# Kernel tuning notes

Hardware: AMD Instinct MI355X
Metric: run time of the kernel (lower is better)

Reference implementation:

```python
import jax, jax.numpy as jnp
import numpy as np
import math

N_EMBD = 1024
HIDDEN = 4 * N_EMBD
N_EXPERTS = 8
TOP_K = 2
B, T = 4, 2048


def new_gelu(x):
    c = math.sqrt(2.0 / math.pi)
    return 0.5 * x * (1.0 + jnp.tanh(c * (x + 0.044715 * x * x * x)))


def setup_inputs() -> dict:
    key = jax.random.key(0)
    ks = jax.random.split(key, 10)
    s = 0.02
    return {
        "x": jax.random.normal(ks[0], (B, T, N_EMBD), dtype=jnp.float32),
        # shared expert (1 shared expert)
        "Wfc_s": jax.random.normal(ks[1], (N_EMBD, HIDDEN), dtype=jnp.float32) * s,
        "bfc_s": jnp.zeros((HIDDEN,), dtype=jnp.float32),
        "Wproj_s": jax.random.normal(ks[2], (HIDDEN, N_EMBD), dtype=jnp.float32) * s,
        "bproj_s": jnp.zeros((N_EMBD,), dtype=jnp.float32),
        # router (no bias)
        "Wr": jax.random.normal(ks[3], (N_EMBD, N_EXPERTS), dtype=jnp.float32) * s,
        # routed experts, stacked on leading expert dim
        "Wfc": jax.random.normal(ks[4], (N_EXPERTS, N_EMBD, HIDDEN), dtype=jnp.float32) * s,
        "bfc": jnp.zeros((N_EXPERTS, HIDDEN), dtype=jnp.float32),
        "Wproj": jax.random.normal(ks[5], (N_EXPERTS, HIDDEN, N_EMBD), dtype=jnp.float32) * s,
        "bproj": jnp.zeros((N_EXPERTS, N_EMBD), dtype=jnp.float32),
    }


def _moe_forward(x, Wfc_s, bfc_s, Wproj_s, bproj_s, Wr, Wfc, bfc, Wproj, bproj):
    Bb, Tt, C = x.shape
    xf = x.reshape(Bb * Tt, C)  # [N, C]
    N = Bb * Tt

    # shared path (1 shared expert, divided by count == 1)
    shared = new_gelu(xf @ Wfc_s + bfc_s) @ Wproj_s + bproj_s

    # router
    logits = xf @ Wr                              # [N, E]
    probs = jax.nn.softmax(logits, axis=-1)
    topk_p, topk_i = jax.lax.top_k(probs, TOP_K)  # [N, K]
    topk_p = topk_p / jnp.sum(topk_p, axis=-1, keepdims=True)

    # dense combine weights: gate[n, e] = normalized prob if expert e selected else 0
    gate = jnp.zeros((N, N_EXPERTS), dtype=xf.dtype)
    gate = gate.at[jnp.arange(N)[:, None], topk_i].add(topk_p)

    routed = jnp.zeros_like(xf)
    for e in range(N_EXPERTS):  # small fixed loop over experts
        h = new_gelu(xf @ Wfc[e] + bfc[e]) @ Wproj[e] + bproj[e]
        routed = routed + h * gate[:, e:e + 1]

    return (shared + routed).reshape(Bb, Tt, C)


def reference(x, Wfc_s, bfc_s, Wproj_s, bproj_s, Wr, Wfc, bfc, Wproj, bproj):
    return _moe_forward(x, Wfc_s, bfc_s, Wproj_s, bproj_s, Wr, Wfc, bfc, Wproj, bproj)
```

## Files before the change

kernel.cpp:

```cpp
#include <hip/hip_runtime.h>
#include <stdint.h>

#define N_TOK 8192
#define C_DIM 1024
#define H_DIM 4096
#define N_EXP 8

typedef __bf16 bf16x8 __attribute__((ext_vector_type(8)));
typedef float floatx4 __attribute__((ext_vector_type(4)));

__device__ __forceinline__ short f2b(float f) {
    unsigned u = __float_as_uint(f);
    unsigned r = (u + 0x7FFFu + ((u >> 16) & 1u)) >> 16;
    return (short)(r & 0xFFFFu);
}

__device__ __forceinline__ float gelu_f(float x) {
    const float c = 0.7978845608028654f;
    float u = c * (x + 0.044715f * x * x * x);
    float a = fabsf(u);
    float e = __expf(-2.0f * a);
    float t = (1.0f - e) / (1.0f + e);
    return 0.5f * x * (1.0f + copysignf(t, u));
}

__global__ void cast_x_k(const float* __restrict__ in, short* __restrict__ out) {
    int i = (blockIdx.x * 256 + threadIdx.x) * 4;
    float4 v = *(const float4*)(in + i);
    short4 o;
    o.x = f2b(v.x); o.y = f2b(v.y); o.z = f2b(v.z); o.w = f2b(v.w);
    *(short4*)(out + i) = o;
}

__global__ void transpose_cast_k(const float* __restrict__ W, short* __restrict__ WT,
                                 int K, int N) {
    __shared__ float tile[32][33];
    size_t moff = (size_t)blockIdx.z * (size_t)K * (size_t)N;
    int n0 = blockIdx.x * 32, k0 = blockIdx.y * 32;
    int tx = threadIdx.x, ty = threadIdx.y;
#pragma unroll
    for (int j = 0; j < 32; j += 8)
        tile[ty + j][tx] = W[moff + (size_t)(k0 + ty + j) * N + n0 + tx];
    __syncthreads();
#pragma unroll
    for (int j = 0; j < 32; j += 8)
        WT[moff + (size_t)(n0 + ty + j) * K + k0 + tx] = f2b(tile[tx][ty + j]);
}

__global__ void router_k(const float* __restrict__ x, const float* __restrict__ Wr,
                         int* __restrict__ counts, int* __restrict__ tok_list,
                         float* __restrict__ gate_list, int* __restrict__ ent) {
    int token = blockIdx.x * 4 + (threadIdx.x >> 6);
    int lane = threadIdx.x & 63;
    const float* xr = x + (size_t)token * C_DIM;
    float p[8];
#pragma unroll
    for (int e = 0; e < 8; ++e) p[e] = 0.f;
    for (int jj = 0; jj < 4; ++jj) {
        int c = (jj * 64 + lane) * 4;
        float4 xv = *(const float4*)(xr + c);
        const float* w = Wr + (size_t)c * 8;
        float xs[4] = {xv.x, xv.y, xv.z, xv.w};
#pragma unroll
        for (int q = 0; q < 4; ++q)
#pragma unroll
            for (int e = 0; e < 8; ++e) p[e] += xs[q] * w[q * 8 + e];
    }
#pragma unroll
    for (int e = 0; e < 8; ++e)
#pragma unroll
        for (int off = 32; off > 0; off >>= 1) p[e] += __shfl_down(p[e], off);
    if (lane == 0) {
        float mx = p[0];
#pragma unroll
        for (int e = 1; e < 8; ++e) mx = fmaxf(mx, p[e]);
        float ex[8];
#pragma unroll
        for (int e = 0; e < 8; ++e) ex[e] = __expf(p[e] - mx);
        int i1 = 0;
#pragma unroll
        for (int e = 1; e < 8; ++e) if (ex[e] > ex[i1]) i1 = e;
        int i2 = (i1 == 0) ? 1 : 0;
#pragma unroll
        for (int e = 0; e < 8; ++e) if (e != i1 && ex[e] > ex[i2]) i2 = e;
        float s2 = ex[i1] + ex[i2];
        float g1 = ex[i1] / s2, g2 = ex[i2] / s2;
        int pos1 = atomicAdd(&counts[i1], 1);
        tok_list[i1 * N_TOK + pos1] = token;
        gate_list[i1 * N_TOK + pos1] = g1;
        ent[token * 2] = (i1 << 16) | pos1;
        int pos2 = atomicAdd(&counts[i2], 1);
        tok_list[i2 * N_TOK + pos2] = token;
        gate_list[i2 * N_TOK + pos2] = g2;
        ent[token * 2 + 1] = (i2 << 16) | pos2;
    }
}

__global__ void offsets_k(const int* __restrict__ counts, int* __restrict__ offs) {
    if (threadIdx.x == 0) {
        int a = 0;
        for (int e = 0; e < 8; ++e) { offs[e] = a; a += counts[e]; }
    }
}

template <int MODE>
__global__ __launch_bounds__(256) void gemm_k(
    const short* __restrict__ Abase, const short* __restrict__ Bbase,
    const float* __restrict__ biasbase, void* __restrict__ OutP,
    const int* __restrict__ counts, const int* __restrict__ offsets,
    const int* __restrict__ tok_base, const float* __restrict__ gate_base,
    int Mconst, int K, int N) {
    const int e = blockIdx.z;
    const int count = counts ? counts[e] : Mconst;
    const int mt = blockIdx.y;
    if (mt * 128 >= count) return;
    const int off = offsets ? offsets[e] : 0;
    const int n0 = blockIdx.x * 128, m0 = mt * 128;
    const short* Bm = Bbase + (size_t)e * (size_t)K * (size_t)N;
    const float* bias = biasbase + (size_t)e * (size_t)N;
    const int tid = threadIdx.x;
    const int sr = tid >> 2, sq = tid & 3;

    __shared__ __align__(16) short As[128 * 56];
    __shared__ __align__(16) short Bs[128 * 56];

    int am0 = m0 + sr, am1 = m0 + sr + 64;
    int cm0 = min(am0, count - 1), cm1 = min(am1, count - 1);
    size_t ga0, ga1;
    if (MODE == 0) {
        if (tok_base) {
            const int* list = tok_base + e * N_TOK;
            ga0 = (size_t)list[cm0];
            ga1 = (size_t)list[cm1];
        } else {
            ga0 = (size_t)cm0; ga1 = (size_t)cm1;
        }
    } else if (MODE == 1) {
        ga0 = (size_t)cm0; ga1 = (size_t)cm1;
    } else {
        ga0 = (size_t)(off + cm0); ga1 = (size_t)(off + cm1);
    }
    const int4* aptr0 = (const int4*)(Abase + ga0 * K + sq * 8);
    const int4* aptr1 = (const int4*)(Abase + ga1 * K + sq * 8);
    const int4* bptr0 = (const int4*)(Bm + (size_t)(n0 + sr) * K + sq * 8);
    const int4* bptr1 = (const int4*)(Bm + (size_t)(n0 + sr + 64) * K + sq * 8);
    int4* asw0 = (int4*)&As[sr * 56 + sq * 8];
    int4* asw1 = (int4*)&As[(sr + 64) * 56 + sq * 8];
    int4* bsw0 = (int4*)&Bs[sr * 56 + sq * 8];
    int4* bsw1 = (int4*)&Bs[(sr + 64) * 56 + sq * 8];

    const int wave = tid >> 6, lane = tid & 63;
    const int wm = (wave >> 1) * 64, wn = (wave & 1) * 64;
    const int fr = lane & 15, quad = lane >> 4;
    const short* ard[4];
    const short* brd[4];
#pragma unroll
    for (int i = 0; i < 4; ++i) {
        ard[i] = &As[(wm + i * 16 + fr) * 56 + quad * 8];
        brd[i] = &Bs[(wn + i * 16 + fr) * 56 + quad * 8];
    }

    floatx4 acc[4][4];
#pragma unroll
    for (int i = 0; i < 4; ++i)
#pragma unroll
        for (int j = 0; j < 4; ++j) acc[i][j] = (floatx4){0.f, 0.f, 0.f, 0.f};

    const int kIters = K / 32;
    for (int kk = 0; kk < kIters; ++kk) {
        int4 av0 = *aptr0; aptr0 += 4;
        int4 av1 = *aptr1; aptr1 += 4;
        int4 bv0 = *bptr0; bptr0 += 4;
        int4 bv1 = *bptr1; bptr1 += 4;
        __syncthreads();
        *asw0 = av0; *asw1 = av1; *bsw0 = bv0; *bsw1 = bv1;
        __syncthreads();
        bf16x8 af[4], bfv[4];
#pragma unroll
        for (int i = 0; i < 4; ++i) af[i] = *(const bf16x8*)ard[i];
#pragma unroll
        for (int j = 0; j < 4; ++j) bfv[j] = *(const bf16x8*)brd[j];
#pragma unroll
        for (int i = 0; i < 4; ++i)
#pragma unroll
            for (int j = 0; j < 4; ++j)
                acc[i][j] = __builtin_amdgcn_mfma_f32_16x16x32_bf16(af[i], bfv[j], acc[i][j], 0, 0, 0);
    }

    float bcol[4];
#pragma unroll
    for (int j = 0; j < 4; ++j) bcol[j] = bias[n0 + wn + j * 16 + fr];

    if (MODE == 0) {
        short* H = (short*)OutP;
#pragma unroll
        for (int i = 0; i < 4; ++i) {
            int mb = m0 + wm + i * 16 + quad * 4;
#pragma unroll
            for (int r = 0; r < 4; ++r) {
                int m = mb + r;
                if (m < count) {
                    size_t row = (size_t)(off + m) * (size_t)N;
#pragma unroll
                    for (int j = 0; j < 4; ++j) {
                        float v = acc[i][j][r] + bcol[j];
                        H[row + n0 + wn + j * 16 + fr] = f2b(gelu_f(v));
                    }
                }
            }
        }
    } else if (MODE == 1) {
        float* O = (float*)OutP;
#pragma unroll
        for (int i = 0; i < 4; ++i) {
            int mb = m0 + wm + i * 16 + quad * 4;
#pragma unroll
            for (int r = 0; r < 4; ++r) {
                int m = mb + r;
                size_t row = (size_t)m * (size_t)N;
#pragma unroll
                for (int j = 0; j < 4; ++j) {
                    O[row + n0 + wn + j * 16 + fr] = acc[i][j][r] + bcol[j];
                }
            }
        }
    } else {
        float* R = (float*)OutP;
        const float* gate = gate_base + e * N_TOK;
#pragma unroll
        for (int i = 0; i < 4; ++i) {
            int mb = m0 + wm + i * 16 + quad * 4;
#pragma unroll
            for (int r = 0; r < 4; ++r) {
                int m = mb + r;
                if (m < count) {
                    float g = gate[m];
                    size_t row = (size_t)(off + m) * (size_t)N;
#pragma unroll
                    for (int j = 0; j < 4; ++j) {
                        float v = acc[i][j][r] + bcol[j];
                        R[row + n0 + wn + j * 16 + fr] = g * v;
                    }
                }
            }
        }
    }
}

__global__ void combine_k(float* __restrict__ out, const float* __restrict__ rout,
                          const int* __restrict__ ent, const int* __restrict__ offs) {
    int idx = blockIdx.x * 256 + threadIdx.x;
    int t = idx >> 8;
    int c4 = (idx & 255) * 4;
    int p0 = ent[t * 2], p1 = ent[t * 2 + 1];
    int m0 = offs[p0 >> 16] + (p0 & 0xFFFF);
    int m1 = offs[p1 >> 16] + (p1 & 0xFFFF);
    float4 o = *(float4*)(out + (size_t)t * 1024 + c4);
    float4 a = *(const float4*)(rout + (size_t)m0 * 1024 + c4);
    float4 b = *(const float4*)(rout + (size_t)m1 * 1024 + c4);
    o.x += a.x + b.x; o.y += a.y + b.y; o.z += a.z + b.z; o.w += a.w + b.w;
    *(float4*)(out + (size_t)t * 1024 + c4) = o;
}

extern "C" void kernel_launch(void* const* d_in, const int* in_sizes, int n_in,
                              void* d_out, int out_size, void* d_ws, size_t ws_size,
                              hipStream_t stream) {
    const float* x       = (const float*)d_in[0];
    const float* Wfc_s   = (const float*)d_in[1];
    const float* bfc_s   = (const float*)d_in[2];
    const float* Wproj_s = (const float*)d_in[3];
    const float* bproj_s = (const float*)d_in[4];
    const float* Wr      = (const float*)d_in[5];
    const float* Wfc     = (const float*)d_in[6];
    const float* bfc     = (const float*)d_in[7];
    const float* Wproj   = (const float*)d_in[8];
    const float* bproj   = (const float*)d_in[9];
    float* out = (float*)d_out;

    char* p = (char*)d_ws;
    short* xb      = (short*)p; p += (size_t)N_TOK * C_DIM * 2;
    short* WfcsT   = (short*)p; p += (size_t)C_DIM * H_DIM * 2;
    short* WprojsT = (short*)p; p += (size_t)C_DIM * H_DIM * 2;
    short* WfcT    = (short*)p; p += (size_t)N_EXP * C_DIM * H_DIM * 2;
    short* WprojT  = (short*)p; p += (size_t)N_EXP * C_DIM * H_DIM * 2;
    short* h       = (short*)p; p += (size_t)2 * N_TOK * H_DIM * 2;
    float* rout    = (float*)p; p += (size_t)2 * N_TOK * C_DIM * 4;
    int*   counts  = (int*)p;   p += 128;
    int*   offs    = (int*)p;   p += 128;
    int*   tok_list  = (int*)p;   p += (size_t)N_EXP * N_TOK * 4;
    float* gate_list = (float*)p; p += (size_t)N_EXP * N_TOK * 4;
    int*   ent     = (int*)p;   p += (size_t)N_TOK * 2 * 4;

    hipMemsetAsync(counts, 0, 32, stream);
    cast_x_k<<<8192, 256, 0, stream>>>(x, xb);
    transpose_cast_k<<<dim3(128, 32, 1), dim3(32, 8), 0, stream>>>(Wfc_s, WfcsT, 1024, 4096);
    transpose_cast_k<<<dim3(32, 128, 1), dim3(32, 8), 0, stream>>>(Wproj_s, WprojsT, 4096, 1024);
    transpose_cast_k<<<dim3(128, 32, 8), dim3(32, 8), 0, stream>>>(Wfc, WfcT, 1024, 4096);
    transpose_cast_k<<<dim3(32, 128, 8), dim3(32, 8), 0, stream>>>(Wproj, WprojT, 4096, 1024);
    router_k<<<2048, 256, 0, stream>>>(x, Wr, counts, tok_list, gate_list, ent);
    offsets_k<<<1, 64, 0, stream>>>(counts, offs);

    gemm_k<0><<<dim3(32, 64, 1), 256, 0, stream>>>(xb, WfcsT, bfc_s, h,
                                                   nullptr, nullptr, nullptr, nullptr,
                                                   8192, C_DIM, H_DIM);
    gemm_k<1><<<dim3(8, 64, 1), 256, 0, stream>>>(h, WprojsT, bproj_s, out,
                                                  nullptr, nullptr, nullptr, nullptr,
                                                  8192, H_DIM, C_DIM);
    gemm_k<0><<<dim3(32, 64, 8), 256, 0, stream>>>(xb, WfcT, bfc, h,
                                                   counts, offs, tok_list, nullptr,
                                                   8192, C_DIM, H_DIM);
    gemm_k<2><<<dim3(8, 64, 8), 256, 0, stream>>>(h, WprojT, bproj, rout,
                                                  counts, offs, nullptr, gate_list,
                                                  8192, H_DIM, C_DIM);
    combine_k<<<8192, 256, 0, stream>>>(out, rout, ent, offs);
}
```

Measured before the change: 1.324 ms.

## Load GEMM tiles directly to LDS with XOR swizzle and grouped tile order

The GEMM tile loads now use global_load_lds (16-byte direct global-to-LDS) instead of staging through registers. The padded LDS layout is replaced by an unpadded 32-column layout with an XOR swizzle on the source chunk, which keeps MFMA fragment reads free of bank conflicts. Block indices are also remapped so groups of 8 M-tiles sweep across N-tiles, which should improve L2 reuse of weight tiles. The loop is still single-buffered, so correctness depends on the barrier waiting for the LDS DMA to finish, and the remap assumes the M grid dimension is a multiple of 8.

```diff
diff --git a/kernel.cpp b/kernel.cpp
--- a/kernel.cpp
+++ b/kernel.cpp
@@ -22,6 +22,12 @@
     float e = __expf(-2.0f * a);
     float t = (1.0f - e) / (1.0f + e);
     return 0.5f * x * (1.0f + copysignf(t, u));
+}
+
+__device__ __forceinline__ void gl_lds16(const short* g, short* l) {
+    __builtin_amdgcn_global_load_lds(
+        (const __attribute__((address_space(1))) unsigned int*)g,
+        (__attribute__((address_space(3))) unsigned int*)l, 16, 0, 0);
 }
 
 __global__ void cast_x_k(const float* __restrict__ in, short* __restrict__ out) {
@@ -103,6 +109,7 @@
     }
 }
 
+#define SWZ(r) (((r) ^ ((r) >> 2)) & 3)
 template <int MODE>
 __global__ __launch_bounds__(256) void gemm_k(
     const short* __restrict__ Abase, const short* __restrict__ Bbase,
@@ -112,52 +119,62 @@
     int Mconst, int K, int N) {
     const int e = blockIdx.z;
     const int count = counts ? counts[e] : Mconst;
-    const int mt = blockIdx.y;
+    const int nTiles = gridDim.x;
+    int bid = blockIdx.y * nTiles + blockIdx.x;
+    const int perGroup = 8 * nTiles;
+    int group = bid / perGroup;
+    int rem = bid - group * perGroup;
+    const int mt = group * 8 + (rem & 7);
+    const int nt = rem >> 3;
     if (mt * 128 >= count) return;
     const int off = offsets ? offsets[e] : 0;
-    const int n0 = blockIdx.x * 128, m0 = mt * 128;
+    const int n0 = nt * 128, m0 = mt * 128;
     const short* Bm = Bbase + (size_t)e * (size_t)K * (size_t)N;
     const float* bias = biasbase + (size_t)e * (size_t)N;
     const int tid = threadIdx.x;
-    const int sr = tid >> 2, sq = tid & 3;
-
-    __shared__ __align__(16) short As[128 * 56];
-    __shared__ __align__(16) short Bs[128 * 56];
-
-    int am0 = m0 + sr, am1 = m0 + sr + 64;
-    int cm0 = min(am0, count - 1), cm1 = min(am1, count - 1);
+    const int wave = tid >> 6, lane = tid & 63;
+
+    __shared__ __align__(16) short As[128 * 32];
+    __shared__ __align__(16) short Bs[128 * 32];
+
+    const int r0 = wave * 32 + (lane >> 2), r1 = r0 + 16;
+    const int ca0 = ((lane & 3) ^ SWZ(r0)) * 8;
+    const int ca1 = ((lane & 3) ^ SWZ(r1)) * 8;
+
+    int am0 = min(m0 + r0, count - 1), am1 = min(m0 + r1, count - 1);
     size_t ga0, ga1;
     if (MODE == 0) {
         if (tok_base) {
             const int* list = tok_base + e * N_TOK;
-            ga0 = (size_t)list[cm0];
-            ga1 = (size_t)list[cm1];
+            ga0 = (size_t)list[am0];
+            ga1 = (size_t)list[am1];
         } else {
-            ga0 = (size_t)cm0; ga1 = (size_t)cm1;
+            ga0 = (size_t)am0; ga1 = (size_t)am1;
         }
     } else if (MODE == 1) {
-        ga0 = (size_t)cm0; ga1 = (size_t)cm1;
+        ga0 = (size_t)am0; ga1 = (size_t)am1;
     } else {
-        ga0 = (size_t)(off + cm0); ga1 = (size_t)(off + cm1);
-    }
-    const int4* aptr0 = (const int4*)(Abase + ga0 * K + sq * 8);
-    const int4* aptr1 = (const int4*)(Abase + ga1 * K + sq * 8);
-    const int4* bptr0 = (const int4*)(Bm + (size_t)(n0 + sr) * K + sq * 8);
-    const int4* bptr1 = (const int4*)(Bm + (size_t)(n0 + sr + 64) * K + sq * 8);
-    int4* asw0 = (int4*)&As[sr * 56 + sq * 8];
-    int4* asw1 = (int4*)&As[(sr + 64) * 56 + sq * 8];
-    int4* bsw0 = (int4*)&Bs[sr * 56 + sq * 8];
-    int4* bsw1 = (int4*)&Bs[(sr + 64) * 56 + sq * 8];
-
-    const int wave = tid >> 6, lane = tid & 63;
+        ga0 = (size_t)(off + am0); ga1 = (size_t)(off + am1);
+    }
+    const short* agp0 = Abase + ga0 * K + ca0;
+    const short* agp1 = Abase + ga1 * K + ca1;
+    const short* bgp0 = Bm + (size_t)(n0 + r0) * K + ca0;
+    const short* bgp1 = Bm + (size_t)(n0 + r1) * K + ca1;
+    short* asw0 = &As[(wave * 32) * 32];
+    short* asw1 = &As[(wave * 32 + 16) * 32];
+    short* bsw0 = &Bs[(wave * 32) * 32];
+    short* bsw1 = &Bs[(wave * 32 + 16) * 32];
+
     const int wm = (wave >> 1) * 64, wn = (wave & 1) * 64;
     const int fr = lane & 15, quad = lane >> 4;
     const short* ard[4];
     const short* brd[4];
 #pragma unroll
     for (int i = 0; i < 4; ++i) {
-        ard[i] = &As[(wm + i * 16 + fr) * 56 + quad * 8];
-        brd[i] = &Bs[(wn + i * 16 + fr) * 56 + quad * 8];
+        int ra = wm + i * 16 + fr;
+        int rb = wn + i * 16 + fr;
+        ard[i] = &As[ra * 32 + ((quad ^ SWZ(ra)) << 3)];
+        brd[i] = &Bs[rb * 32 + ((quad ^ SWZ(rb)) << 3)];
     }
 
     floatx4 acc[4][4];
@@ -168,12 +185,12 @@
 
     const int kIters = K / 32;
     for (int kk = 0; kk < kIters; ++kk) {
-        int4 av0 = *aptr0; aptr0 += 4;
-        int4 av1 = *aptr1; aptr1 += 4;
-        int4 bv0 = *bptr0; bptr0 += 4;
-        int4 bv1 = *bptr1; bptr1 += 4;
         __syncthreads();
-        *asw0 = av0; *asw1 = av1; *bsw0 = bv0; *bsw1 = bv1;
+        gl_lds16(agp0, asw0);
+        gl_lds16(agp1, asw1);
+        gl_lds16(bgp0, bsw0);
+        gl_lds16(bgp1, bsw1);
+        agp0 += 32; agp1 += 32; bgp0 += 32; bgp1 += 32;
         __syncthreads();
         bf16x8 af[4], bfv[4];
 #pragma unroll
```

Result: no change. 1.317 ms (-0.5%).
